# Kernel tuning notes

Hardware: AMD Instinct MI355X
Metric: run time of the kernel (lower is better)

The kernel has to match this reference:

```python
import jax, jax.numpy as jnp
import numpy as np

N = 500_000   # total nodes
D = 256       # in_dim
G = 1024      # num graphs (segments)
H = max(32, D // 2)  # gate hidden = 128
L = D // 2    # local pool dim = 128


def setup_inputs() -> dict:
    key = jax.random.key(0)
    ks = jax.random.split(key, 8)
    x = jax.random.normal(ks[0], (N, D), dtype=jnp.float32)
    batch = jnp.sort(jax.random.randint(ks[1], (N,), 0, G, dtype=jnp.int32))
    s = 0.02
    w1 = jax.random.normal(ks[2], (D, H), dtype=jnp.float32) * s
    b1 = jnp.zeros((H,), dtype=jnp.float32)
    w2 = jax.random.normal(ks[3], (H, 1), dtype=jnp.float32) * s
    b2 = jnp.zeros((1,), dtype=jnp.float32)
    lp_w = jax.random.normal(ks[4], (D, L), dtype=jnp.float32) * s
    lp_b = jnp.zeros((L,), dtype=jnp.float32)
    return {"x": x, "batch": batch, "w1": w1, "b1": b1, "w2": w2,
            "b2": b2, "lp_w": lp_w, "lp_b": lp_b}


def reference(x, batch, w1, b1, w2, b2, lp_w, lp_b):
    # segment counts (guard empty segments)
    ones = jnp.ones((x.shape[0],), dtype=x.dtype)
    cnt = jax.ops.segment_sum(ones, batch, num_segments=G)
    cnt = jnp.maximum(cnt, 1.0)[:, None]                      # [G,1]

    # mean pool
    mean_p = jax.ops.segment_sum(x, batch, num_segments=G) / cnt

    # max pool
    max_p = jax.ops.segment_max(x, batch, num_segments=G)

    # global attention pool: gate MLP -> per-segment softmax -> weighted sum
    # (Dropout is identity at inference.)
    h = jax.nn.gelu(x @ w1 + b1, approximate=False)           # [N,H]
    gate = (h @ w2 + b2)[:, 0]                                # [N]
    gmax = jax.ops.segment_max(gate, batch, num_segments=G)   # [G]
    e = jnp.exp(gate - gmax[batch])                           # [N]
    denom = jax.ops.segment_sum(e, batch, num_segments=G)     # [G]
    a = e / denom[batch]                                      # [N] softmax per graph
    att_p = jax.ops.segment_sum(a[:, None] * x, batch, num_segments=G)

    # local MLP pool then mean
    local = jax.nn.gelu(x @ lp_w + lp_b, approximate=False)   # [N,L]
    local_mean = jax.ops.segment_sum(local, batch, num_segments=G) / cnt

    return jnp.concatenate([mean_p, max_p, att_p, local_mean], axis=-1)  # [G, 3D + D//2]
```

## Files before the change

kernel.cpp:

```cpp
#include <hip/hip_runtime.h>
#include <hip/hip_bf16.h>
#include <float.h>
#include <math.h>


typedef __bf16 bf16;
typedef __bf16 bf16x8 __attribute__((ext_vector_type(8)));
typedef float f32x4 __attribute__((ext_vector_type(4)));

#define D 256
#define HDIM 128
#define LDIM 128
#define ROWS 48
#define XPAD 260
#define NMT 3

__device__ __forceinline__ float gelu_f(float v) {
    return 0.5f * v * (1.0f + erff(v * 0.70710678118654752f));
}

__global__ __launch_bounds__(256) void k_prep(const float* __restrict__ w1,
                                              const float* __restrict__ lpw,
                                              bf16* __restrict__ w1T,
                                              bf16* __restrict__ lpT) {
    int t = blockIdx.x * 256 + threadIdx.x;
    if (t < HDIM * D) {
        int n = t >> 8;
        int k = t & 255;
        w1T[t] = (bf16)w1[k * HDIM + n];
        lpT[t] = (bf16)lpw[k * LDIM + n];
    }
}

__device__ __forceinline__ int lower_bound_i(const int* a, int n, int v) {
    int lo = 0, hi = n;
    while (lo < hi) { int mid = (lo + hi) >> 1; if (a[mid] < v) lo = mid + 1; else hi = mid; }
    return lo;
}

__global__ __launch_bounds__(256, 3) void k_fused(
    const float* __restrict__ x, const int* __restrict__ batch,
    const bf16* __restrict__ w1T, const float* __restrict__ b1,
    const float* __restrict__ w2, const float* __restrict__ b2,
    const bf16* __restrict__ lpT, const float* __restrict__ lpb,
    float* __restrict__ out, int N)
{
    __shared__ float xs[ROWS][XPAD];
    __shared__ float gpart[4][64];
    __shared__ int sse[2];

    const int g    = blockIdx.x;
    const int tid  = threadIdx.x;
    const int wave = tid >> 6;
    const int lane = tid & 63;
    const int quad = lane >> 4;
    const int l16  = lane & 15;

    if (tid == 0) sse[0] = lower_bound_i(batch, N, g);
    if (tid == 1) sse[1] = lower_bound_i(batch, N, g + 1);
    __syncthreads();
    const int start = sse[0], end = sse[1];
    const int cnt = end - start;

    const int c0 = wave * 32 + l16;
    const int c1 = c0 + 16;
    const float b1c0 = b1[c0], b1c1 = b1[c1];
    const float w2c0 = w2[c0], w2c1 = w2[c1];
    const float lb0  = lpb[c0], lb1 = lpb[c1];
    const float b2c  = b2[0];

    float msum0=0.f, msum1=0.f, msum2=0.f, msum3=0.f;
    float mmax0=-FLT_MAX, mmax1=-FLT_MAX, mmax2=-FLT_MAX, mmax3=-FLT_MAX;
    float asum0=0.f, asum1=0.f, asum2=0.f, asum3=0.f;
    float ls0=0.f, ls1=0.f;
    float m_run = -FLT_MAX, denom = 0.f;

    const f32x4 zf = {0.f, 0.f, 0.f, 0.f};

    for (int base = start; base < end; base += ROWS) {
        const int vr = min(ROWS, end - base);
        const float* xb = x + (long)base * D + (lane << 2);

        if (vr == ROWS) {
            #pragma unroll
            for (int it = 0; it < 12; ++it) {
                const int row = it * 4 + wave;
                const float4 t4 = *(const float4*)(xb + row * D);
                msum0 += t4.x; msum1 += t4.y; msum2 += t4.z; msum3 += t4.w;
                mmax0 = fmaxf(mmax0, t4.x); mmax1 = fmaxf(mmax1, t4.y);
                mmax2 = fmaxf(mmax2, t4.z); mmax3 = fmaxf(mmax3, t4.w);
                f32x4 v; v[0]=t4.x; v[1]=t4.y; v[2]=t4.z; v[3]=t4.w;
                *(f32x4*)(&xs[row][lane << 2]) = v;
            }
        } else {
            #pragma unroll
            for (int it = 0; it < 12; ++it) {
                const int row = it * 4 + wave;
                f32x4 v = zf;
                if (row < vr) {
                    const float4 t4 = *(const float4*)(xb + row * D);
                    msum0 += t4.x; msum1 += t4.y; msum2 += t4.z; msum3 += t4.w;
                    mmax0 = fmaxf(mmax0, t4.x); mmax1 = fmaxf(mmax1, t4.y);
                    mmax2 = fmaxf(mmax2, t4.z); mmax3 = fmaxf(mmax3, t4.w);
                    v[0]=t4.x; v[1]=t4.y; v[2]=t4.z; v[3]=t4.w;
                }
                *(f32x4*)(&xs[row][lane << 2]) = v;
            }
        }
        __syncthreads();

        f32x4 h0[NMT], h1[NMT], l0[NMT], l1[NMT];
        #pragma unroll
        for (int mt = 0; mt < NMT; ++mt) { h0[mt]=zf; h1[mt]=zf; l0[mt]=zf; l1[mt]=zf; }

        #pragma unroll
        for (int kt = 0; kt < 8; ++kt) {
            const int k0 = kt * 32 + quad * 8;
            const bf16x8 bw0 = *(const bf16x8*)(w1T + c0 * D + k0);
            const bf16x8 bw1 = *(const bf16x8*)(w1T + c1 * D + k0);
            const bf16x8 bp0 = *(const bf16x8*)(lpT + c0 * D + k0);
            const bf16x8 bp1 = *(const bf16x8*)(lpT + c1 * D + k0);
            #pragma unroll
            for (int mt = 0; mt < NMT; ++mt) {
                const float* xp = &xs[mt * 16 + l16][k0];
                const f32x4 fa = *(const f32x4*)(xp);
                const f32x4 fb = *(const f32x4*)(xp + 4);
                bf16x8 a;
                a[0]=(bf16)fa[0]; a[1]=(bf16)fa[1]; a[2]=(bf16)fa[2]; a[3]=(bf16)fa[3];
                a[4]=(bf16)fb[0]; a[5]=(bf16)fb[1]; a[6]=(bf16)fb[2]; a[7]=(bf16)fb[3];
                h0[mt] = __builtin_amdgcn_mfma_f32_16x16x32_bf16(a, bw0, h0[mt], 0, 0, 0);
                h1[mt] = __builtin_amdgcn_mfma_f32_16x16x32_bf16(a, bw1, h1[mt], 0, 0, 0);
                l0[mt] = __builtin_amdgcn_mfma_f32_16x16x32_bf16(a, bp0, l0[mt], 0, 0, 0);
                l1[mt] = __builtin_amdgcn_mfma_f32_16x16x32_bf16(a, bp1, l1[mt], 0, 0, 0);
            }
        }

        #pragma unroll
        for (int mt = 0; mt < NMT; ++mt) {
            #pragma unroll
            for (int r = 0; r < 4; ++r) {
                float v = gelu_f(h0[mt][r] + b1c0) * w2c0
                        + gelu_f(h1[mt][r] + b1c1) * w2c1;
                v += __shfl_down(v, 8, 16);
                v += __shfl_down(v, 4, 16);
                v += __shfl_down(v, 2, 16);
                v += __shfl_down(v, 1, 16);
                if (l16 == 0) gpart[wave][mt * 16 + quad * 4 + r] = v;
            }
        }
        __syncthreads();

        float gv = -FLT_MAX;
        if (lane < vr)
            gv = gpart[0][lane] + gpart[1][lane] + gpart[2][lane] + gpart[3][lane] + b2c;
        float cm = gv;
        #pragma unroll
        for (int off = 32; off > 0; off >>= 1) cm = fmaxf(cm, __shfl_xor(cm, off));
        const float m_new = fmaxf(m_run, cm);
        const float fr = expf(m_run - m_new);
        const float ew = (lane < vr) ? expf(gv - m_new) : 0.f;
        float se = ew;
        #pragma unroll
        for (int off = 32; off > 0; off >>= 1) se += __shfl_xor(se, off);
        denom = denom * fr + se;
        m_run = m_new;

        if (vr == ROWS) {
            #pragma unroll
            for (int mt = 0; mt < NMT; ++mt)
                #pragma unroll
                for (int r = 0; r < 4; ++r) {
                    ls0 += gelu_f(l0[mt][r] + lb0);
                    ls1 += gelu_f(l1[mt][r] + lb1);
                }
        } else {
            #pragma unroll
            for (int mt = 0; mt < NMT; ++mt)
                #pragma unroll
                for (int r = 0; r < 4; ++r) {
                    if (mt * 16 + quad * 4 + r < vr) {
                        ls0 += gelu_f(l0[mt][r] + lb0);
                        ls1 += gelu_f(l1[mt][r] + lb1);
                    }
                }
        }

        asum0 *= fr; asum1 *= fr; asum2 *= fr; asum3 *= fr;
        #pragma unroll
        for (int it = 0; it < 12; ++it) {
            const int row = it * 4 + wave;
            const float e = __shfl(ew, row);
            const f32x4 v = *(const f32x4*)(&xs[row][lane << 2]);
            asum0 += e * v[0]; asum1 += e * v[1];
            asum2 += e * v[2]; asum3 += e * v[3];
        }
        __syncthreads();
    }

    ls0 += __shfl_xor(ls0, 16); ls0 += __shfl_xor(ls0, 32);
    ls1 += __shfl_xor(ls1, 16); ls1 += __shfl_xor(ls1, 32);

    const float inv  = 1.0f / fmaxf((float)cnt, 1.0f);
    const float invd = (denom > 0.f) ? 1.0f / denom : 0.f;
    const long  o    = (long)g * 896;

    float* red = &xs[0][0];
    const int cb = (wave << 8) + (lane << 2);
    red[cb]        = msum0; red[cb+1]        = msum1; red[cb+2]        = msum2; red[cb+3]        = msum3;
    red[1024 + cb] = asum0; red[1024 + cb+1] = asum1; red[1024 + cb+2] = asum2; red[1024 + cb+3] = asum3;
    red[2048 + cb] = mmax0; red[2048 + cb+1] = mmax1; red[2048 + cb+2] = mmax2; red[2048 + cb+3] = mmax3;
    if (quad == 0) {
        out[o + 768 + c0] = ls0 * inv;
        out[o + 768 + c1] = ls1 * inv;
    }
    __syncthreads();
    {
        const int col = tid;
        const float s = red[col]        + red[256 + col]  + red[512 + col]  + red[768 + col];
        const float a = red[1024 + col] + red[1280 + col] + red[1536 + col] + red[1792 + col];
        float mm = fmaxf(fmaxf(red[2048 + col], red[2304 + col]),
                         fmaxf(red[2560 + col], red[2816 + col]));
        if (cnt == 0) mm = -INFINITY;
        out[o + col]       = s * inv;
        out[o + 256 + col] = mm;
        out[o + 512 + col] = a * invd;
    }
}

extern "C" void kernel_launch(void* const* d_in, const int* in_sizes, int n_in,
                              void* d_out, int out_size, void* d_ws, size_t ws_size,
                              hipStream_t stream) {
    const float* x   = (const float*)d_in[0];
    const int* batch = (const int*)d_in[1];
    const float* w1  = (const float*)d_in[2];
    const float* b1  = (const float*)d_in[3];
    const float* w2  = (const float*)d_in[4];
    const float* b2  = (const float*)d_in[5];
    const float* lpw = (const float*)d_in[6];
    const float* lpb = (const float*)d_in[7];
    float* out = (float*)d_out;

    const int N = in_sizes[0] / D;
    const int G = out_size / 896;

    char* ws = (char*)d_ws;
    bf16* w1T = (bf16*)ws;
    bf16* lpT = (bf16*)(ws + (size_t)HDIM * D * sizeof(bf16));

    k_prep<<<(HDIM * D + 255) / 256, 256, 0, stream>>>(w1, lpw, w1T, lpT);
    k_fused<<<G, 256, 0, stream>>>(x, batch, w1T, b1, w2, b2, lpT, lpb, out, N);
}
```

Baseline: 1.036 ms.

## Split each segment across four blocks with partial-softmax merge kernel and bf16 LDS tile

Each graph segment is now processed by four blocks instead of one, and a new merge kernel combines the partial sums, maxes, attention sums and local sums using log-sum-exp rescaling. A separate boundaries kernel replaces the per-block binary search. The x tile is kept in registers for the attention and mean accumulations, while LDS stores a bf16 copy so the MFMA loop no longer converts fp32 to bf16, and the trailing barrier per tile is dropped. The goal is more blocks to fill the device (1024 blocks is only a few per CU) and less LDS traffic. The cost is two extra kernel launches, workspace traffic for the partials, and higher register pressure from holding 12 float4 values.

After: 1.082 ms. 1.04x slower.

```diff
diff --git a/kernel.cpp b/kernel.cpp
--- a/kernel.cpp
+++ b/kernel.cpp
@@ -5,6 +5,7 @@
 
 
 typedef __bf16 bf16;
+typedef __bf16 bf16x4 __attribute__((ext_vector_type(4)));
 typedef __bf16 bf16x8 __attribute__((ext_vector_type(8)));
 typedef float f32x4 __attribute__((ext_vector_type(4)));
 
@@ -12,8 +13,9 @@
 #define HDIM 128
 #define LDIM 128
 #define ROWS 48
-#define XPAD 260
+#define XCOL 264
 #define NMT 3
+#define SPLIT 4
 
 __device__ __forceinline__ float gelu_f(float v) {
     return 0.5f * v * (1.0f + erff(v * 0.70710678118654752f));
@@ -32,35 +34,50 @@
     }
 }
 
-__device__ __forceinline__ int lower_bound_i(const int* a, int n, int v) {
-    int lo = 0, hi = n;
-    while (lo < hi) { int mid = (lo + hi) >> 1; if (a[mid] < v) lo = mid + 1; else hi = mid; }
-    return lo;
-}
-
-__global__ __launch_bounds__(256, 3) void k_fused(
-    const float* __restrict__ x, const int* __restrict__ batch,
-    const bf16* __restrict__ w1T, const float* __restrict__ b1,
-    const float* __restrict__ w2, const float* __restrict__ b2,
-    const bf16* __restrict__ lpT, const float* __restrict__ lpb,
-    float* __restrict__ out, int N)
+__global__ __launch_bounds__(256) void k_bounds(const int* __restrict__ batch,
+                                                int* __restrict__ segstart,
+                                                int N, int G) {
+    int i = blockIdx.x * 256 + threadIdx.x;
+    if (i >= N) return;
+    int b = batch[i];
+    if (i == 0) {
+        for (int g = 0; g <= b; ++g) segstart[g] = 0;
+    } else {
+        int p = batch[i - 1];
+        for (int g = p + 1; g <= b; ++g) segstart[g] = i;
+    }
+    if (i == N - 1) {
+        for (int g = b + 1; g <= G; ++g) segstart[g] = N;
+    }
+}
+
+__global__ __launch_bounds__(256) __attribute__((amdgpu_waves_per_eu(3, 3)))
+void k_fused(const float* __restrict__ x, const int* __restrict__ segstart,
+             const bf16* __restrict__ w1T, const float* __restrict__ b1,
+             const float* __restrict__ w2, const float* __restrict__ b2,
+             const bf16* __restrict__ lpT, const float* __restrict__ lpb,
+             float* __restrict__ psum, float* __restrict__ pmax,
+             float* __restrict__ patt, float* __restrict__ pls,
+             float* __restrict__ pscal)
 {
-    __shared__ float xs[ROWS][XPAD];
+    __shared__ bf16  xs[ROWS][XCOL];
     __shared__ float gpart[4][64];
-    __shared__ int sse[2];
-
-    const int g    = blockIdx.x;
+    __shared__ float red[3][4][256];
+
+    const int blk  = blockIdx.x;
+    const int g    = blk >> 2;
+    const int part = blk & 3;
     const int tid  = threadIdx.x;
     const int wave = tid >> 6;
     const int lane = tid & 63;
     const int quad = lane >> 4;
     const int l16  = lane & 15;
 
-    if (tid == 0) sse[0] = lower_bound_i(batch, N, g);
-    if (tid == 1) sse[1] = lower_bound_i(batch, N, g + 1);
-    __syncthreads();
-    const int start = sse[0], end = sse[1];
-    const int cnt = end - start;
+    const int gs = segstart[g], ge = segstart[g + 1];
+    const int cnt = ge - gs;
+    const int per = (cnt + SPLIT - 1) >> 2;
+    const int start = gs + part * per;
+    const int end   = min(start + per, ge);
 
     const int c0 = wave * 32 + l16;
     const int c1 = c0 + 16;
@@ -68,6 +85,10 @@
     const float w2c0 = w2[c0], w2c1 = w2[c1];
     const float lb0  = lpb[c0], lb1 = lpb[c1];
     const float b2c  = b2[0];
+    const bf16* wb0 = w1T + c0 * D;
+    const bf16* wb1 = w1T + c1 * D;
+    const bf16* pb0 = lpT + c0 * D;
+    const bf16* pb1 = lpT + c1 * D;
 
     float msum0=0.f, msum1=0.f, msum2=0.f, msum3=0.f;
     float mmax0=-FLT_MAX, mmax1=-FLT_MAX, mmax2=-FLT_MAX, mmax3=-FLT_MAX;
@@ -81,31 +102,41 @@
         const int vr = min(ROWS, end - base);
         const float* xb = x + (long)base * D + (lane << 2);
 
+        float4 xr[12];
         if (vr == ROWS) {
+            #pragma unroll
+            for (int it = 0; it < 12; ++it)
+                xr[it] = *(const float4*)(xb + (it * 4 + wave) * D);
+            #pragma unroll
+            for (int it = 0; it < 12; ++it) {
+                msum0 += xr[it].x; msum1 += xr[it].y;
+                msum2 += xr[it].z; msum3 += xr[it].w;
+                mmax0 = fmaxf(mmax0, xr[it].x); mmax1 = fmaxf(mmax1, xr[it].y);
+                mmax2 = fmaxf(mmax2, xr[it].z); mmax3 = fmaxf(mmax3, xr[it].w);
+            }
+        } else {
             #pragma unroll
             for (int it = 0; it < 12; ++it) {
                 const int row = it * 4 + wave;
-                const float4 t4 = *(const float4*)(xb + row * D);
-                msum0 += t4.x; msum1 += t4.y; msum2 += t4.z; msum3 += t4.w;
-                mmax0 = fmaxf(mmax0, t4.x); mmax1 = fmaxf(mmax1, t4.y);
-                mmax2 = fmaxf(mmax2, t4.z); mmax3 = fmaxf(mmax3, t4.w);
-                f32x4 v; v[0]=t4.x; v[1]=t4.y; v[2]=t4.z; v[3]=t4.w;
-                *(f32x4*)(&xs[row][lane << 2]) = v;
-            }
-        } else {
+                xr[it] = make_float4(0.f, 0.f, 0.f, 0.f);
+                if (row < vr) xr[it] = *(const float4*)(xb + row * D);
+            }
             #pragma unroll
             for (int it = 0; it < 12; ++it) {
-                const int row = it * 4 + wave;
-                f32x4 v = zf;
-                if (row < vr) {
-                    const float4 t4 = *(const float4*)(xb + row * D);
-                    msum0 += t4.x; msum1 += t4.y; msum2 += t4.z; msum3 += t4.w;
-                    mmax0 = fmaxf(mmax0, t4.x); mmax1 = fmaxf(mmax1, t4.y);
-                    mmax2 = fmaxf(mmax2, t4.z); mmax3 = fmaxf(mmax3, t4.w);
-                    v[0]=t4.x; v[1]=t4.y; v[2]=t4.z; v[3]=t4.w;
+                if (it * 4 + wave < vr) {
+                    msum0 += xr[it].x; msum1 += xr[it].y;
+                    msum2 += xr[it].z; msum3 += xr[it].w;
+                    mmax0 = fmaxf(mmax0, xr[it].x); mmax1 = fmaxf(mmax1, xr[it].y);
+                    mmax2 = fmaxf(mmax2, xr[it].z); mmax3 = fmaxf(mmax3, xr[it].w);
                 }
-                *(f32x4*)(&xs[row][lane << 2]) = v;
-            }
+            }
+        }
+        #pragma unroll
+        for (int it = 0; it < 12; ++it) {
+            bf16x4 pk;
+            pk[0] = (bf16)xr[it].x; pk[1] = (bf16)xr[it].y;
+            pk[2] = (bf16)xr[it].z; pk[3] = (bf16)xr[it].w;
+            *(bf16x4*)(&xs[it * 4 + wave][lane << 2]) = pk;
         }
         __syncthreads();
 
@@ -116,18 +147,13 @@
         #pragma unroll
         for (int kt = 0; kt < 8; ++kt) {
             const int k0 = kt * 32 + quad * 8;
-            const bf16x8 bw0 = *(const bf16x8*)(w1T + c0 * D + k0);
-            const bf16x8 bw1 = *(const bf16x8*)(w1T + c1 * D + k0);
-            const bf16x8 bp0 = *(const bf16x8*)(lpT + c0 * D + k0);
-            const bf16x8 bp1 = *(const bf16x8*)(lpT + c1 * D + k0);
+            const bf16x8 bw0 = *(const bf16x8*)(wb0 + k0);
+            const bf16x8 bw1 = *(const bf16x8*)(wb1 + k0);
+            const bf16x8 bp0 = *(const bf16x8*)(pb0 + k0);
+            const bf16x8 bp1 = *(const bf16x8*)(pb1 + k0);
             #pragma unroll
             for (int mt = 0; mt < NMT; ++mt) {
-                const float* xp = &xs[mt * 16 + l16][k0];
-                const f32x4 fa = *(const f32x4*)(xp);
-                const f32x4 fb = *(const f32x4*)(xp + 4);
-                bf16x8 a;
-                a[0]=(bf16)fa[0]; a[1]=(bf16)fa[1]; a[2]=(bf16)fa[2]; a[3]=(bf16)fa[3];
-                a[4]=(bf16)fb[0]; a[5]=(bf16)fb[1]; a[6]=(bf16)fb[2]; a[7]=(bf16)fb[3];
+                const bf16x8 a = *(const bf16x8*)(&xs[mt * 16 + l16][k0]);
                 h0[mt] = __builtin_amdgcn_mfma_f32_16x16x32_bf16(a, bw0, h0[mt], 0, 0, 0);
                 h1[mt] = __builtin_amdgcn_mfma_f32_16x16x32_bf16(a, bw1, h1[mt], 0, 0, 0);
                 l0[mt] = __builtin_amdgcn_mfma_f32_16x16x32_bf16(a, bp0, l0[mt], 0, 0, 0);
@@ -188,42 +214,90 @@
         asum0 *= fr; asum1 *= fr; asum2 *= fr; asum3 *= fr;
         #pragma unroll
         for (int it = 0; it < 12; ++it) {
-            const int row = it * 4 + wave;
-            const float e = __shfl(ew, row);
-            const f32x4 v = *(const f32x4*)(&xs[row][lane << 2]);
-            asum0 += e * v[0]; asum1 += e * v[1];
-            asum2 += e * v[2]; asum3 += e * v[3];
-        }
-        __syncthreads();
+            const float e = __shfl(ew, it * 4 + wave);
+            asum0 += e * xr[it].x; asum1 += e * xr[it].y;
+            asum2 += e * xr[it].z; asum3 += e * xr[it].w;
+        }
     }
 
     ls0 += __shfl_xor(ls0, 16); ls0 += __shfl_xor(ls0, 32);
     ls1 += __shfl_xor(ls1, 16); ls1 += __shfl_xor(ls1, 32);
 
-    const float inv  = 1.0f / fmaxf((float)cnt, 1.0f);
-    const float invd = (denom > 0.f) ? 1.0f / denom : 0.f;
-    const long  o    = (long)g * 896;
-
-    float* red = &xs[0][0];
-    const int cb = (wave << 8) + (lane << 2);
-    red[cb]        = msum0; red[cb+1]        = msum1; red[cb+2]        = msum2; red[cb+3]        = msum3;
-    red[1024 + cb] = asum0; red[1024 + cb+1] = asum1; red[1024 + cb+2] = asum2; red[1024 + cb+3] = asum3;
-    red[2048 + cb] = mmax0; red[2048 + cb+1] = mmax1; red[2048 + cb+2] = mmax2; red[2048 + cb+3] = mmax3;
+    f32x4 v0 = {msum0, msum1, msum2, msum3};
+    f32x4 v1 = {mmax0, mmax1, mmax2, mmax3};
+    f32x4 v2 = {asum0, asum1, asum2, asum3};
+    *(f32x4*)(&red[0][wave][lane << 2]) = v0;
+    *(f32x4*)(&red[1][wave][lane << 2]) = v1;
+    *(f32x4*)(&red[2][wave][lane << 2]) = v2;
     if (quad == 0) {
-        out[o + 768 + c0] = ls0 * inv;
-        out[o + 768 + c1] = ls1 * inv;
+        pls[(long)blk * LDIM + c0] = ls0;
+        pls[(long)blk * LDIM + c1] = ls1;
+    }
+    if (tid == 0) {
+        const int pcnt = (end > start) ? (end - start) : 0;
+        pscal[(long)blk * 4 + 0] = m_run;
+        pscal[(long)blk * 4 + 1] = denom;
+        pscal[(long)blk * 4 + 2] = (float)pcnt;
     }
     __syncthreads();
     {
         const int col = tid;
-        const float s = red[col]        + red[256 + col]  + red[512 + col]  + red[768 + col];
-        const float a = red[1024 + col] + red[1280 + col] + red[1536 + col] + red[1792 + col];
-        float mm = fmaxf(fmaxf(red[2048 + col], red[2304 + col]),
-                         fmaxf(red[2560 + col], red[2816 + col]));
-        if (cnt == 0) mm = -INFINITY;
+        const float s  = red[0][0][col] + red[0][1][col] + red[0][2][col] + red[0][3][col];
+        const float mx = fmaxf(fmaxf(red[1][0][col], red[1][1][col]),
+                               fmaxf(red[1][2][col], red[1][3][col]));
+        const float a  = red[2][0][col] + red[2][1][col] + red[2][2][col] + red[2][3][col];
+        psum[(long)blk * 256 + col] = s;
+        pmax[(long)blk * 256 + col] = mx;
+        patt[(long)blk * 256 + col] = a;
+    }
+}
+
+__global__ __launch_bounds__(256) void k_merge(
+    const float* __restrict__ psum, const float* __restrict__ pmax,
+    const float* __restrict__ patt, const float* __restrict__ pls,
+    const float* __restrict__ pscal, float* __restrict__ out)
+{
+    const int g   = blockIdx.x;
+    const int tid = threadIdx.x;
+    __shared__ float sm[SPLIT], sd[SPLIT], sc[SPLIT];
+    if (tid < SPLIT) {
+        sm[tid] = pscal[(long)(g * SPLIT + tid) * 4 + 0];
+        sd[tid] = pscal[(long)(g * SPLIT + tid) * 4 + 1];
+        sc[tid] = pscal[(long)(g * SPLIT + tid) * 4 + 2];
+    }
+    __syncthreads();
+    const float M   = fmaxf(fmaxf(sm[0], sm[1]), fmaxf(sm[2], sm[3]));
+    const float cnt = sc[0] + sc[1] + sc[2] + sc[3];
+    float w[SPLIT];
+    float denom = 0.f;
+    #pragma unroll
+    for (int p = 0; p < SPLIT; ++p) {
+        w[p] = expf(sm[p] - M);
+        denom += sd[p] * w[p];
+    }
+    const float inv  = 1.0f / fmaxf(cnt, 1.0f);
+    const float invd = (denom > 0.f) ? 1.0f / denom : 0.f;
+    const long  o    = (long)g * 896;
+    const long  pb   = (long)g * SPLIT * 256;
+    {
+        const int col = tid;
+        float s = 0.f, a = 0.f, mx = -FLT_MAX;
+        #pragma unroll
+        for (int p = 0; p < SPLIT; ++p) {
+            s += psum[pb + p * 256 + col];
+            mx = fmaxf(mx, pmax[pb + p * 256 + col]);
+            a += patt[pb + p * 256 + col] * w[p];
+        }
         out[o + col]       = s * inv;
-        out[o + 256 + col] = mm;
+        out[o + 256 + col] = (cnt > 0.f) ? mx : -INFINITY;
         out[o + 512 + col] = a * invd;
+    }
+    if (tid < 128) {
+        const long lb = (long)g * SPLIT * 128;
+        float s = 0.f;
+        #pragma unroll
+        for (int p = 0; p < SPLIT; ++p) s += pls[lb + p * 128 + tid];
+        out[o + 768 + tid] = s * inv;
     }
 }
 
@@ -242,11 +316,23 @@
 
     const int N = in_sizes[0] / D;
     const int G = out_size / 896;
+    const int NB = SPLIT * G;
 
     char* ws = (char*)d_ws;
-    bf16* w1T = (bf16*)ws;
-    bf16* lpT = (bf16*)(ws + (size_t)HDIM * D * sizeof(bf16));
+    size_t off = 0;
+    auto alloc = [&](size_t bytes) { void* p = ws + off; off = (off + bytes + 255) & ~(size_t)255; return p; };
+    bf16*  w1T      = (bf16*)alloc((size_t)HDIM * D * sizeof(bf16));
+    bf16*  lpT      = (bf16*)alloc((size_t)LDIM * D * sizeof(bf16));
+    int*   segstart = (int*)alloc((size_t)(G + 1) * sizeof(int));
+    float* psum     = (float*)alloc((size_t)NB * 256 * sizeof(float));
+    float* pmax     = (float*)alloc((size_t)NB * 256 * sizeof(float));
+    float* patt     = (float*)alloc((size_t)NB * 256 * sizeof(float));
+    float* pls      = (float*)alloc((size_t)NB * 128 * sizeof(float));
+    float* pscal    = (float*)alloc((size_t)NB * 4 * sizeof(float));
 
     k_prep<<<(HDIM * D + 255) / 256, 256, 0, stream>>>(w1, lpw, w1T, lpT);
-    k_fused<<<G, 256, 0, stream>>>(x, batch, w1T, b1, w2, b2, lpT, lpb, out, N);
-}
+    k_bounds<<<(N + 255) / 256, 256, 0, stream>>>(batch, segstart, N, G);
+    k_fused<<<NB, 256, 0, stream>>>(x, segstart, w1T, b1, w2, b2, lpT, lpb,
+                                    psum, pmax, patt, pls, pscal);
+    k_merge<<<G, 256, 0, stream>>>(psum, pmax, patt, pls, pscal, out);
+}
```
